# Performance work log

Measured on AMD Instinct MI355X. Metric: run time of the kernel, lower is better.

Reference implementation:

```python
import jax, jax.numpy as jnp
import numpy as np

EPS = 1e-5  # haiku LayerNorm default
BIG = 1e9


def layernorm(x, scale, offset):
    mu = jnp.mean(x, axis=-1, keepdims=True)
    var = jnp.var(x, axis=-1, keepdims=True)
    return scale * (x - mu) * jax.lax.rsqrt(var + EPS) + offset


def setup_inputs() -> dict:
    key = jax.random.key(0)
    ks = iter(jax.random.split(key, 32))
    N_res, N_tok, C, H = 4096, 512, 384, 8
    kd = C // H  # 48, key_dim and value_dim per head
    F = 4 * C    # transition hidden
    s = 0.02
    inp = {
        "original": jax.random.normal(next(ks), (1, N_res, C), jnp.float32),
        "resampled": jax.random.normal(next(ks), (1, N_tok, C), jnp.float32),
        "attention_mask": (jax.random.uniform(next(ks), (H, N_tok, N_res)) < 0.9).astype(jnp.float32),
        "output_mask": jnp.ones((1, N_tok), jnp.float32),
        "input_mask": jnp.ones((1, N_res), jnp.float32),
        # cross-attention LayerNorms
        "qn_scale": jnp.ones((C,), jnp.float32), "qn_offset": jnp.zeros((C,), jnp.float32),
        "dn_scale": jnp.ones((C,), jnp.float32), "dn_offset": jnp.zeros((C,), jnp.float32),
        # attention projections
        "query_w": jax.random.normal(next(ks), (C, H, kd), jnp.float32) * s,
        "key_w": jax.random.normal(next(ks), (C, H, kd), jnp.float32) * s,
        "value_w": jax.random.normal(next(ks), (C, H, kd), jnp.float32) * s,
        "gating_w": jax.random.normal(next(ks), (C, H, kd), jnp.float32) * s,
        "gating_b": jnp.ones((H, kd), jnp.float32),
        "output_w": jax.random.normal(next(ks), (H, kd, C), jnp.float32) * s,
        "output_b": jnp.zeros((C,), jnp.float32),
        # resampled transition
        "rt_ln_scale": jnp.ones((C,), jnp.float32), "rt_ln_offset": jnp.zeros((C,), jnp.float32),
        "rt_w1": jax.random.normal(next(ks), (C, F), jnp.float32) * s, "rt_b1": jnp.zeros((F,), jnp.float32),
        "rt_w2": jax.random.normal(next(ks), (F, C), jnp.float32) * s, "rt_b2": jnp.zeros((C,), jnp.float32),
        # original transition
        "ot_ln_scale": jnp.ones((C,), jnp.float32), "ot_ln_offset": jnp.zeros((C,), jnp.float32),
        "ot_w1": jax.random.normal(next(ks), (C, F), jnp.float32) * s, "ot_b1": jnp.zeros((F,), jnp.float32),
        "ot_w2": jax.random.normal(next(ks), (F, C), jnp.float32) * s, "ot_b2": jnp.zeros((C,), jnp.float32),
    }
    return inp


def reference(original, resampled, attention_mask, output_mask, input_mask,
              qn_scale, qn_offset, dn_scale, dn_offset,
              query_w, key_w, value_w, gating_w, gating_b, output_w, output_b,
              rt_ln_scale, rt_ln_offset, rt_w1, rt_b1, rt_w2, rt_b2,
              ot_ln_scale, ot_ln_offset, ot_w1, ot_b1, ot_w2, ot_b2):
    # ---- CrossAttention (deterministic; dropout rate 0) ----
    bias = BIG * (attention_mask - 1.0)          # [H, T, R]
    q_in = layernorm(resampled, qn_scale, qn_offset)   # [1, T, C]
    d_in = layernorm(original, dn_scale, dn_offset)    # [1, R, C]
    kd = query_w.shape[-1]
    q = jnp.einsum('bqa,ahc->bqhc', q_in, query_w) * kd ** (-0.5)
    k = jnp.einsum('bka,ahc->bkhc', d_in, key_w)
    v = jnp.einsum('bka,ahc->bkhc', d_in, value_w)
    logits = jnp.einsum('bqhc,bkhc->bhqk', q, k) + bias[None]  # [1, H, T, R]
    weights = jax.nn.softmax(logits, axis=-1)
    weighted_avg = jnp.einsum('bhqk,bkhc->bqhc', weights, v)
    gate = jax.nn.sigmoid(jnp.einsum('bqc,chv->bqhv', q_in, gating_w) + gating_b)
    weighted_avg = weighted_avg * gate
    attn_out = jnp.einsum('bqhc,hco->bqo', weighted_avg, output_w) + output_b
    resampled = resampled + attn_out             # residual (dropout off)
    # ---- resampled Transition + residual ----
    t = layernorm(resampled, rt_ln_scale, rt_ln_offset)
    t = jax.nn.relu(t @ rt_w1 + rt_b1) @ rt_w2 + rt_b2
    resampled = resampled + t
    # ---- original Transition + residual ----
    t = layernorm(original, ot_ln_scale, ot_ln_offset)
    t = jax.nn.relu(t @ ot_w1 + ot_b1) @ ot_w2 + ot_b2
    original = original + t
    return resampled.astype(jnp.float32), original.astype(jnp.float32)
```

## Files before the change

kernel.cpp:

```cpp
#include <hip/hip_runtime.h>
#include <hip/hip_bf16.h>
#include <cstdint>

typedef unsigned short u16;
typedef __attribute__((ext_vector_type(8))) __bf16 bf16x8;
typedef __attribute__((ext_vector_type(4))) float f32x4;
typedef __attribute__((ext_vector_type(4))) short s16x4;

__device__ __forceinline__ u16 f2bf(float f) {
  union { float f; unsigned u; } v; v.f = f;
  unsigned r = (v.u + 0x7FFFu + ((v.u >> 16) & 1u)) >> 16;
  return (u16)r;
}

__device__ __forceinline__ void gll16(const u16* gp, u16* lp) {
  auto g1 = reinterpret_cast<const __attribute__((address_space(1))) void*>(
      reinterpret_cast<uintptr_t>(gp));
  auto l3 = reinterpret_cast<__attribute__((address_space(3))) void*>(
      reinterpret_cast<uintptr_t>(lp));
  __builtin_amdgcn_global_load_lds(g1, l3, 16, 0, 0);
}

__global__ __launch_bounds__(128) void ln_kernel(
    const float* __restrict__ x,
    const float* __restrict__ s1, const float* __restrict__ o1, u16* __restrict__ y1,
    const float* __restrict__ s2, const float* __restrict__ o2, u16* __restrict__ y2) {
  const int row = blockIdx.x;
  const int t = threadIdx.x;
  const float* xr = x + (size_t)row * 384;
  float v0 = xr[t], v1 = xr[t + 128], v2 = xr[t + 256];
  float sum = v0 + v1 + v2;
  float sq = v0 * v0 + v1 * v1 + v2 * v2;
#pragma unroll
  for (int off = 32; off > 0; off >>= 1) {
    sum += __shfl_xor(sum, off);
    sq += __shfl_xor(sq, off);
  }
  __shared__ float red[4];
  if ((t & 63) == 0) { red[(t >> 6) * 2] = sum; red[(t >> 6) * 2 + 1] = sq; }
  __syncthreads();
  sum = red[0] + red[2];
  sq = red[1] + red[3];
  const float mu = sum * (1.f / 384.f);
  const float rstd = rsqrtf(sq * (1.f / 384.f) - mu * mu + 1e-5f);
#pragma unroll
  for (int j = 0; j < 3; ++j) {
    const int cc = t + 128 * j;
    const float xv = (j == 0 ? v0 : (j == 1 ? v1 : v2));
    const float xn = (xv - mu) * rstd;
    y1[(size_t)row * 384 + cc] = f2bf(s1[cc] * xn + o1[cc]);
    if (y2) y2[(size_t)row * 384 + cc] = f2bf(s2[cc] * xn + o2[cc]);
  }
}

struct TBatch {
  const float* in[9];
  u16* out[9];
  int K[9], N[9];
  float scale[9];
  int boff[10];
};

__global__ __launch_bounds__(256) void transpose_all(TBatch tb) {
  __shared__ float tile[32][33];
  const int bid = blockIdx.x;
  int j = 0;
  while (j < 8 && bid >= tb.boff[j + 1]) ++j;
  const int lb = bid - tb.boff[j];
  const int NB = tb.N[j] >> 5;
  const int bx = lb % NB, by = lb / NB;
  const float* in = tb.in[j];
  u16* out = tb.out[j];
  const int K = tb.K[j], N = tb.N[j];
  const float scale = tb.scale[j];
  const int tx = threadIdx.x, ty = threadIdx.y;
  const int nb = bx * 32, kb = by * 32;
#pragma unroll
  for (int i = 0; i < 4; ++i)
    tile[ty + 8 * i][tx] = in[(size_t)(kb + ty + 8 * i) * N + nb + tx];
  __syncthreads();
#pragma unroll
  for (int i = 0; i < 4; ++i)
    out[(size_t)(nb + ty + 8 * i) * K + kb + tx] = f2bf(tile[tx][ty + 8 * i] * scale);
}

struct GArgs {
  const u16* A; const u16* Bt;
  int M, N, K;
  const float* bias; const float* bias2; const float* residual;
  float* outf; u16* outb; u16* outb2;
};

template <int BM, int BN, int EPI>
__global__ __launch_bounds__(256, (BM == 128 ? 2 : 4)) void gemm_bt(GArgs g) {
  constexpr int MT = BM / 32, NT = BN / 32;
  const int tid = threadIdx.x;
  const int w = tid >> 6;
  const int lane = tid & 63;
  const int gq = lane >> 4, c = lane & 15;
  const int brow = blockIdx.y * BM, bcol = blockIdx.x * BN;
  const int wm = (w >> 1) * (BM / 2), wn = (w & 1) * (BN / 2);
  __shared__ u16 As[2][BM][64];
  __shared__ u16 Bs[2][BN][64];
  const int K = g.K;

  f32x4 acc[MT][NT];
#pragma unroll
  for (int mt = 0; mt < MT; ++mt)
#pragma unroll
    for (int nt = 0; nt < NT; ++nt)
#pragma unroll
      for (int r = 0; r < 4; ++r) acc[mt][nt][r] = 0.f;

  const int srow = lane >> 3;
  const int schunk = (lane & 7) ^ srow;
  const u16* aSrc = g.A + (size_t)(brow + w * (BM / 4) + srow) * K + schunk * 8;
  const u16* bSrc = g.Bt + (size_t)(bcol + w * (BN / 4) + srow) * K + schunk * 8;

  auto STAGE = [&](int buf, int k0) {
#pragma unroll
    for (int i = 0; i < BM / 32; ++i)
      gll16(aSrc + (size_t)(8 * i) * K + k0, &As[buf][w * (BM / 4) + i * 8][0]);
#pragma unroll
    for (int i = 0; i < BN / 32; ++i)
      gll16(bSrc + (size_t)(8 * i) * K + k0, &Bs[buf][w * (BN / 4) + i * 8][0]);
  };

  auto COMPUTE = [&](int buf) {
#pragma unroll
    for (int ks = 0; ks < 2; ++ks) {
      bf16x8 af[MT], bfv[NT];
#pragma unroll
      for (int mt = 0; mt < MT; ++mt) {
        const int row = wm + mt * 16 + c;
        const int ch = ((ks << 2) | gq) ^ (row & 7);
        af[mt] = *(const bf16x8*)&As[buf][row][ch * 8];
      }
#pragma unroll
      for (int nt = 0; nt < NT; ++nt) {
        const int row = wn + nt * 16 + c;
        const int ch = ((ks << 2) | gq) ^ (row & 7);
        bfv[nt] = *(const bf16x8*)&Bs[buf][row][ch * 8];
      }
#pragma unroll
      for (int mt = 0; mt < MT; ++mt)
#pragma unroll
        for (int nt = 0; nt < NT; ++nt)
          acc[mt][nt] =
              __builtin_amdgcn_mfma_f32_16x16x32_bf16(af[mt], bfv[nt], acc[mt][nt], 0, 0, 0);
    }
  };

  const int NTILES = K >> 6;
  STAGE(0, 0);
  __syncthreads();
  int cur = 0;
  for (int t = 0; t < NTILES; ++t) {
    if (t + 1 < NTILES) STAGE(cur ^ 1, (t + 1) << 6);
    COMPUTE(cur);
    __syncthreads();
    cur ^= 1;
  }

  const int N = g.N;
#pragma unroll
  for (int mt = 0; mt < MT; ++mt) {
#pragma unroll
    for (int nt = 0; nt < NT; ++nt) {
      const int n = bcol + wn + nt * 16 + c;
#pragma unroll
      for (int r = 0; r < 4; ++r) {
        const int m = brow + wm + mt * 16 + 4 * gq + r;
        const float v = acc[mt][nt][r];
        if (EPI == 0) {
          g.outb[(size_t)m * N + n] = f2bf(fmaxf(v + g.bias[n], 0.f));
        } else if (EPI == 1) {
          g.outf[(size_t)m * N + n] = v + g.bias[n] + g.residual[(size_t)m * N + n];
        } else if (EPI == 2) {
          if (n < 384) g.outb[(size_t)(n / 48) * 4096 * 48 + (size_t)m * 48 + (n % 48)] = f2bf(v);
          else g.outb2[(size_t)(n - 384) * 4096 + m] = f2bf(v);
        } else {
          if (n < 384) g.outb[(size_t)m * 384 + n] = f2bf(v);
          else {
            const float sg = v + g.bias2[n - 384];
            g.outf[(size_t)m * 384 + (n - 384)] = 1.f / (1.f + __expf(-sg));
          }
        }
      }
    }
  }
}

__global__ __launch_bounds__(512) void attn_kernel(
    const u16* __restrict__ Kh, const u16* __restrict__ Qb, const u16* __restrict__ Vt,
    const float* __restrict__ mask, float* __restrict__ partO, float* __restrict__ partL) {
  const int tid = threadIdx.x;
  const int w = tid >> 6;
  const int lane = tid & 63;
  const int gq = lane >> 4, c = lane & 15;
  const int qt = blockIdx.x, h = blockIdx.y, z = blockIdx.z;
  const int tb = qt * 16;

  bf16x8 zf;
#pragma unroll
  for (int j = 0; j < 8; ++j) zf[j] = (__bf16)0.f;
  f32x4 zero4;
#pragma unroll
  for (int j = 0; j < 4; ++j) zero4[j] = 0.f;

  const u16* qrow = Qb + (size_t)(tb + c) * 384 + h * 48;
  bf16x8 qf0 = *(const bf16x8*)(qrow + 8 * gq);
  bf16x8 qf1 = zf;
  if (gq < 2) qf1 = *(const bf16x8*)(qrow + 32 + 8 * gq);

  float psum = 0.f;
  f32x4 O0 = zero4, O1 = zero4, O2 = zero4;

  const int kb = z * 1024 + w * 128;
  const float* mrow = mask + ((size_t)h * 512 + tb + c) * 4096;
  const u16* khead = Kh + (size_t)h * 4096 * 48;
  const u16* vbase = Vt + (size_t)(h * 48) * 4096;

#pragma unroll
  for (int it = 0; it < 4; ++it) {
    const int rb = kb + it * 32;
    const u16* krow0 = khead + (size_t)(rb + c) * 48;
    const u16* krow1 = krow0 + (size_t)16 * 48;

    bf16x8 kf0a = *(const bf16x8*)(krow0 + 8 * gq);
    bf16x8 kf0b = zf;
    if (gq < 2) kf0b = *(const bf16x8*)(krow0 + 32 + 8 * gq);
    bf16x8 kf1a = *(const bf16x8*)(krow1 + 8 * gq);
    bf16x8 kf1b = zf;
    if (gq < 2) kf1b = *(const bf16x8*)(krow1 + 32 + 8 * gq);

    f32x4 s0 = __builtin_amdgcn_mfma_f32_16x16x32_bf16(kf0a, qf0, zero4, 0, 0, 0);
    s0 = __builtin_amdgcn_mfma_f32_16x16x32_bf16(kf0b, qf1, s0, 0, 0, 0);
    f32x4 s1 = __builtin_amdgcn_mfma_f32_16x16x32_bf16(kf1a, qf0, zero4, 0, 0, 0);
    s1 = __builtin_amdgcn_mfma_f32_16x16x32_bf16(kf1b, qf1, s1, 0, 0, 0);

    const f32x4 mv0 = *(const f32x4*)(mrow + rb + 4 * gq);
    const f32x4 mv1 = *(const f32x4*)(mrow + rb + 16 + 4 * gq);

    float p0[4], p1[4];
#pragma unroll
    for (int r = 0; r < 4; ++r) {
      p0[r] = __expf(s0[r] + 1e9f * (mv0[r] - 1.f));
      p1[r] = __expf(s1[r] + 1e9f * (mv1[r] - 1.f));
      psum += p0[r] + p1[r];
    }

    s16x4 pa0, pa1;
#pragma unroll
    for (int r = 0; r < 4; ++r) {
      pa0[r] = (short)f2bf(p0[r]);
      pa1[r] = (short)f2bf(p1[r]);
    }
#pragma unroll
    for (int nt = 0; nt < 3; ++nt) {
      const u16* vp = vbase + (size_t)(nt * 16 + c) * 4096 + rb + 4 * gq;
      const s16x4 vf0 = *(const s16x4*)(vp);
      const s16x4 vf1 = *(const s16x4*)(vp + 16);
      f32x4& O = (nt == 0 ? O0 : (nt == 1 ? O1 : O2));
      O = __builtin_amdgcn_mfma_f32_16x16x16bf16_1k(pa0, vf0, O, 0, 0, 0);
      O = __builtin_amdgcn_mfma_f32_16x16x16bf16_1k(pa1, vf1, O, 0, 0, 0);
    }
  }

  psum += __shfl_xor(psum, 16);
  psum += __shfl_xor(psum, 32);

  __shared__ float oS[8][16][48];
  __shared__ float lS[8][16];
  if (gq == 0) lS[w][c] = psum;
#pragma unroll
  for (int r = 0; r < 4; ++r) {
    oS[w][4 * gq + r][c] = O0[r];
    oS[w][4 * gq + r][16 + c] = O1[r];
    oS[w][4 * gq + r][32 + c] = O2[r];
  }
  __syncthreads();

  float* pO = partO + (((size_t)z * 32 + qt) * 8 + h) * 768;
  for (int idx = tid; idx < 768; idx += 512) {
    const int q = idx / 48, d = idx % 48;
    float v = 0.f;
#pragma unroll
    for (int ww = 0; ww < 8; ++ww) v += oS[ww][q][d];
    pO[idx] = v;
  }
  if (tid < 16) {
    float L = 0.f;
#pragma unroll
    for (int ww = 0; ww < 8; ++ww) L += lS[ww][tid];
    partL[(((size_t)z * 32 + qt) * 8 + h) * 16 + tid] = L;
  }
}

__global__ __launch_bounds__(256) void attn_merge(
    const float* __restrict__ partO, const float* __restrict__ partL,
    const float* __restrict__ gate, u16* __restrict__ attng) {
  const int qt = blockIdx.x, h = blockIdx.y;
  for (int idx = threadIdx.x; idx < 768; idx += 256) {
    const int q = idx / 48, d = idx % 48;
    float O = 0.f, L = 0.f;
#pragma unroll
    for (int z = 0; z < 4; ++z) {
      O += partO[(((size_t)z * 32 + qt) * 8 + h) * 768 + idx];
      L += partL[(((size_t)z * 32 + qt) * 8 + h) * 16 + q];
    }
    const size_t off = (size_t)(qt * 16 + q) * 384 + h * 48 + d;
    attng[off] = f2bf(O / L * gate[off]);
  }
}

extern "C" void kernel_launch(void* const* d_in, const int* in_sizes, int n_in,
                              void* d_out, int out_size, void* d_ws, size_t ws_size,
                              hipStream_t stream) {
  (void)in_sizes; (void)n_in; (void)out_size; (void)ws_size;
  const float* original = (const float*)d_in[0];
  const float* resampled = (const float*)d_in[1];
  const float* amask = (const float*)d_in[2];
  const float* qn_s = (const float*)d_in[5];
  const float* qn_o = (const float*)d_in[6];
  const float* dn_s = (const float*)d_in[7];
  const float* dn_o = (const float*)d_in[8];
  const float* w_q = (const float*)d_in[9];
  const float* w_k = (const float*)d_in[10];
  const float* w_v = (const float*)d_in[11];
  const float* w_g = (const float*)d_in[12];
  const float* b_g = (const float*)d_in[13];
  const float* w_o = (const float*)d_in[14];
  const float* b_o = (const float*)d_in[15];
  const float* rt_s = (const float*)d_in[16];
  const float* rt_o = (const float*)d_in[17];
  const float* rtw1 = (const float*)d_in[18];
  const float* rtb1 = (const float*)d_in[19];
  const float* rtw2 = (const float*)d_in[20];
  const float* rtb2 = (const float*)d_in[21];
  const float* ot_s = (const float*)d_in[22];
  const float* ot_o = (const float*)d_in[23];
  const float* otw1 = (const float*)d_in[24];
  const float* otb1 = (const float*)d_in[25];
  const float* otw2 = (const float*)d_in[26];
  const float* otb2 = (const float*)d_in[27];

  float* out_res = (float*)d_out;
  float* out_orig = out_res + 512 * 384;

  char* p = (char*)d_ws;
  auto alloc = [&](size_t n) {
    void* r = (void*)p;
    p += (n + 255) & ~(size_t)255;
    return r;
  };
  u16* dinb = (u16*)alloc(4096 * 384 * 2);
  u16* otin = (u16*)alloc(4096 * 384 * 2);
  u16* qin = (u16*)alloc(512 * 384 * 2);
  u16* Kh = (u16*)alloc((size_t)8 * 4096 * 48 * 2);
  u16* Vt = (u16*)alloc(384 * 4096 * 2);
  u16* Qb = (u16*)alloc(512 * 384 * 2);
  float* gateb = (float*)alloc(512 * 384 * 4);
  u16* attng = (u16*)alloc(512 * 384 * 2);
  float* res2 = (float*)alloc(512 * 384 * 4);
  u16* tin = (u16*)alloc(512 * 384 * 2);
  u16* H1 = (u16*)alloc(512 * 1536 * 2);
  u16* H2 = (u16*)alloc((size_t)4096 * 1536 * 2);
  u16* BtKV = (u16*)alloc(768 * 384 * 2);
  u16* BtQG = (u16*)alloc(768 * 384 * 2);
  u16* OwT = (u16*)alloc(384 * 384 * 2);
  u16* Rt1T = (u16*)alloc(1536 * 384 * 2);
  u16* Rt2T = (u16*)alloc(384 * 1536 * 2);
  u16* Ot1T = (u16*)alloc(1536 * 384 * 2);
  u16* Ot2T = (u16*)alloc(384 * 1536 * 2);
  float* partO = (float*)alloc((size_t)4 * 32 * 8 * 768 * 4);
  float* partL = (float*)alloc((size_t)4 * 32 * 8 * 16 * 4);

  {
    TBatch tb{};
    const float qscale = 0.14433756729740643f;
    const float* ins[9] = {w_q, w_g, w_k, w_v, w_o, rtw1, rtw2, otw1, otw2};
    u16* outs[9] = {BtQG, BtQG + 384 * 384, BtKV, BtKV + 384 * 384, OwT,
                    Rt1T, Rt2T, Ot1T, Ot2T};
    const int Ks[9] = {384, 384, 384, 384, 384, 384, 1536, 384, 1536};
    const int Ns[9] = {384, 384, 384, 384, 384, 1536, 384, 1536, 384};
    int off = 0;
    for (int j = 0; j < 9; ++j) {
      tb.in[j] = ins[j]; tb.out[j] = outs[j];
      tb.K[j] = Ks[j]; tb.N[j] = Ns[j];
      tb.scale[j] = (j == 0) ? qscale : 1.f;
      tb.boff[j] = off;
      off += (Ns[j] >> 5) * (Ks[j] >> 5);
    }
    tb.boff[9] = off;
    transpose_all<<<off, dim3(32, 8), 0, stream>>>(tb);
  }

  ln_kernel<<<4096, 128, 0, stream>>>(original, dn_s, dn_o, dinb, ot_s, ot_o, otin);
  ln_kernel<<<512, 128, 0, stream>>>(resampled, qn_s, qn_o, qin, nullptr, nullptr, nullptr);

  {
    GArgs a{};
    a.A = dinb; a.Bt = BtKV; a.M = 4096; a.N = 768; a.K = 384;
    a.outb = Kh; a.outb2 = Vt;
    gemm_bt<128, 128, 2><<<dim3(6, 32), 256, 0, stream>>>(a);
  }
  {
    GArgs a{};
    a.A = qin; a.Bt = BtQG; a.M = 512; a.N = 768; a.K = 384;
    a.outb = Qb; a.outf = gateb; a.bias2 = b_g;
    gemm_bt<64, 64, 3><<<dim3(12, 8), 256, 0, stream>>>(a);
  }

  attn_kernel<<<dim3(32, 8, 4), 512, 0, stream>>>(Kh, Qb, Vt, amask, partO, partL);
  attn_merge<<<dim3(32, 8), 256, 0, stream>>>(partO, partL, gateb, attng);

  {
    GArgs a{};
    a.A = attng; a.Bt = OwT; a.M = 512; a.N = 384; a.K = 384;
    a.bias = b_o; a.residual = resampled; a.outf = res2;
    gemm_bt<64, 64, 1><<<dim3(6, 8), 256, 0, stream>>>(a);
  }
  ln_kernel<<<512, 128, 0, stream>>>(res2, rt_s, rt_o, tin, nullptr, nullptr, nullptr);
  {
    GArgs a{};
    a.A = tin; a.Bt = Rt1T; a.M = 512; a.N = 1536; a.K = 384;
    a.bias = rtb1; a.outb = H1;
    gemm_bt<64, 64, 0><<<dim3(24, 8), 256, 0, stream>>>(a);
  }
  {
    GArgs a{};
    a.A = H1; a.Bt = Rt2T; a.M = 512; a.N = 384; a.K = 1536;
    a.bias = rtb2; a.residual = res2; a.outf = out_res;
    gemm_bt<64, 64, 1><<<dim3(6, 8), 256, 0, stream>>>(a);
  }
  {
    GArgs a{};
    a.A = otin; a.Bt = Ot1T; a.M = 4096; a.N = 1536; a.K = 384;
    a.bias = otb1; a.outb = H2;
    gemm_bt<128, 128, 0><<<dim3(12, 32), 256, 0, stream>>>(a);
  }
  {
    GArgs a{};
    a.A = H2; a.Bt = Ot2T; a.M = 4096; a.N = 384; a.K = 1536;
    a.bias = otb2; a.residual = original; a.outf = out_orig;
    gemm_bt<64, 64, 1><<<dim3(6, 64), 256, 0, stream>>>(a);
  }
}
```

Measured before the change: 292.2 us.

## Split-K FFN down-projections, pad K/Q heads, and restructure attention into 8-way key split

Merges the two input LayerNorm launches into one kernel. Pads K and Q per-head storage to 64 columns, with a memset providing zeros, so the attention kernel drops its conditional half-loads. It also strides V rows by 4160 to avoid bank/channel aliasing. The attention kernel moves to 256 threads with 8 key splits, software-pipelines its loads across iterations, and turns the mask into a multiply on exp instead of a large negative bias. Both transition down-projection GEMMs become split-K with a fused merge kernel that adds bias and residual, raising parallelism at the cost of extra fp32 partial traffic and a memset.

```diff
diff --git a/kernel.cpp b/kernel.cpp
--- a/kernel.cpp
+++ b/kernel.cpp
@@ -6,6 +6,8 @@
 typedef __attribute__((ext_vector_type(8))) __bf16 bf16x8;
 typedef __attribute__((ext_vector_type(4))) float f32x4;
 typedef __attribute__((ext_vector_type(4))) short s16x4;
+
+#define VSTR 4160
 
 __device__ __forceinline__ u16 f2bf(float f) {
   union { float f; unsigned u; } v; v.f = f;
@@ -21,13 +23,15 @@
   __builtin_amdgcn_global_load_lds(g1, l3, 16, 0, 0);
 }
 
-__global__ __launch_bounds__(128) void ln_kernel(
-    const float* __restrict__ x,
-    const float* __restrict__ s1, const float* __restrict__ o1, u16* __restrict__ y1,
-    const float* __restrict__ s2, const float* __restrict__ o2, u16* __restrict__ y2) {
+__global__ __launch_bounds__(128) void ln_all(
+    const float* __restrict__ orig, const float* __restrict__ resam,
+    const float* __restrict__ dn_s, const float* __restrict__ dn_o, u16* __restrict__ dinb,
+    const float* __restrict__ ot_s, const float* __restrict__ ot_o, u16* __restrict__ otin,
+    const float* __restrict__ qn_s, const float* __restrict__ qn_o, u16* __restrict__ qin) {
   const int row = blockIdx.x;
   const int t = threadIdx.x;
-  const float* xr = x + (size_t)row * 384;
+  const bool isOrig = row < 4096;
+  const float* xr = isOrig ? orig + (size_t)row * 384 : resam + (size_t)(row - 4096) * 384;
   float v0 = xr[t], v1 = xr[t + 128], v2 = xr[t + 256];
   float sum = v0 + v1 + v2;
   float sq = v0 * v0 + v1 * v1 + v2 * v2;
@@ -48,8 +52,41 @@
     const int cc = t + 128 * j;
     const float xv = (j == 0 ? v0 : (j == 1 ? v1 : v2));
     const float xn = (xv - mu) * rstd;
-    y1[(size_t)row * 384 + cc] = f2bf(s1[cc] * xn + o1[cc]);
-    if (y2) y2[(size_t)row * 384 + cc] = f2bf(s2[cc] * xn + o2[cc]);
+    if (isOrig) {
+      dinb[(size_t)row * 384 + cc] = f2bf(dn_s[cc] * xn + dn_o[cc]);
+      otin[(size_t)row * 384 + cc] = f2bf(ot_s[cc] * xn + ot_o[cc]);
+    } else {
+      qin[(size_t)(row - 4096) * 384 + cc] = f2bf(qn_s[cc] * xn + qn_o[cc]);
+    }
+  }
+}
+
+__global__ __launch_bounds__(128) void ln_kernel(
+    const float* __restrict__ x,
+    const float* __restrict__ s1, const float* __restrict__ o1, u16* __restrict__ y1) {
+  const int row = blockIdx.x;
+  const int t = threadIdx.x;
+  const float* xr = x + (size_t)row * 384;
+  float v0 = xr[t], v1 = xr[t + 128], v2 = xr[t + 256];
+  float sum = v0 + v1 + v2;
+  float sq = v0 * v0 + v1 * v1 + v2 * v2;
+#pragma unroll
+  for (int off = 32; off > 0; off >>= 1) {
+    sum += __shfl_xor(sum, off);
+    sq += __shfl_xor(sq, off);
+  }
+  __shared__ float red[4];
+  if ((t & 63) == 0) { red[(t >> 6) * 2] = sum; red[(t >> 6) * 2 + 1] = sq; }
+  __syncthreads();
+  sum = red[0] + red[2];
+  sq = red[1] + red[3];
+  const float mu = sum * (1.f / 384.f);
+  const float rstd = rsqrtf(sq * (1.f / 384.f) - mu * mu + 1e-5f);
+#pragma unroll
+  for (int j = 0; j < 3; ++j) {
+    const int cc = t + 128 * j;
+    const float xv = (j == 0 ? v0 : (j == 1 ? v1 : v2));
+    y1[(size_t)row * 384 + cc] = f2bf(s1[cc] * ((xv - mu) * rstd) + o1[cc]);
   }
 }
 
@@ -86,7 +123,7 @@
 
 struct GArgs {
   const u16* A; const u16* Bt;
-  int M, N, K;
+  int M, N, K, Kld;
   const float* bias; const float* bias2; const float* residual;
   float* outf; u16* outb; u16* outb2;
 };
@@ -103,6 +140,8 @@
   __shared__ u16 As[2][BM][64];
   __shared__ u16 Bs[2][BN][64];
   const int K = g.K;
+  const int Kld = g.Kld;
+  const size_t koff = (size_t)blockIdx.z * K;
 
   f32x4 acc[MT][NT];
 #pragma unroll
@@ -114,16 +153,16 @@
 
   const int srow = lane >> 3;
   const int schunk = (lane & 7) ^ srow;
-  const u16* aSrc = g.A + (size_t)(brow + w * (BM / 4) + srow) * K + schunk * 8;
-  const u16* bSrc = g.Bt + (size_t)(bcol + w * (BN / 4) + srow) * K + schunk * 8;
+  const u16* aSrc = g.A + (size_t)(brow + w * (BM / 4) + srow) * Kld + koff + schunk * 8;
+  const u16* bSrc = g.Bt + (size_t)(bcol + w * (BN / 4) + srow) * Kld + koff + schunk * 8;
 
   auto STAGE = [&](int buf, int k0) {
 #pragma unroll
     for (int i = 0; i < BM / 32; ++i)
-      gll16(aSrc + (size_t)(8 * i) * K + k0, &As[buf][w * (BM / 4) + i * 8][0]);
+      gll16(aSrc + (size_t)(8 * i) * Kld + k0, &As[buf][w * (BM / 4) + i * 8][0]);
 #pragma unroll
     for (int i = 0; i < BN / 32; ++i)
-      gll16(bSrc + (size_t)(8 * i) * K + k0, &Bs[buf][w * (BN / 4) + i * 8][0]);
+      gll16(bSrc + (size_t)(8 * i) * Kld + k0, &Bs[buf][w * (BN / 4) + i * 8][0]);
   };
 
   auto COMPUTE = [&](int buf) {
@@ -177,21 +216,89 @@
         } else if (EPI == 1) {
           g.outf[(size_t)m * N + n] = v + g.bias[n] + g.residual[(size_t)m * N + n];
         } else if (EPI == 2) {
-          if (n < 384) g.outb[(size_t)(n / 48) * 4096 * 48 + (size_t)m * 48 + (n % 48)] = f2bf(v);
-          else g.outb2[(size_t)(n - 384) * 4096 + m] = f2bf(v);
-        } else {
-          if (n < 384) g.outb[(size_t)m * 384 + n] = f2bf(v);
+          if (n < 384)
+            g.outb[(size_t)(n / 48) * 4096 * 64 + (size_t)m * 64 + (n % 48)] = f2bf(v);
+          else
+            g.outb2[(size_t)(n - 384) * VSTR + m] = f2bf(v);
+        } else if (EPI == 3) {
+          if (n < 384)
+            g.outb[(size_t)(n / 48) * 512 * 64 + (size_t)m * 64 + (n % 48)] = f2bf(v);
           else {
             const float sg = v + g.bias2[n - 384];
             g.outf[(size_t)m * 384 + (n - 384)] = 1.f / (1.f + __expf(-sg));
           }
+        } else {
+          g.outf[(size_t)blockIdx.z * g.M * N + (size_t)m * N + n] = v;
         }
       }
     }
   }
 }
 
-__global__ __launch_bounds__(512) void attn_kernel(
+struct KIter {
+  bf16x8 kA0, kA1, kB0, kB1;
+  f32x4 mv0, mv1;
+  s16x4 v0, v1, v2, v3, v4, v5;
+};
+
+__device__ __forceinline__ KIter load_iter(const u16* __restrict__ khead,
+                                           const float* __restrict__ mrow,
+                                           const u16* __restrict__ vcol, int rb) {
+  KIter I;
+  const u16* kr = khead + (size_t)rb * 64;
+  I.kA0 = *(const bf16x8*)(kr);
+  I.kA1 = *(const bf16x8*)(kr + 32);
+  I.kB0 = *(const bf16x8*)(kr + 16 * 64);
+  I.kB1 = *(const bf16x8*)(kr + 16 * 64 + 32);
+  I.mv0 = *(const f32x4*)(mrow + rb);
+  I.mv1 = *(const f32x4*)(mrow + rb + 16);
+  const u16* vp0 = vcol + rb;
+  I.v0 = *(const s16x4*)(vp0);
+  I.v1 = *(const s16x4*)(vp0 + 16);
+  const u16* vp1 = vp0 + (size_t)16 * VSTR;
+  I.v2 = *(const s16x4*)(vp1);
+  I.v3 = *(const s16x4*)(vp1 + 16);
+  const u16* vp2 = vp1 + (size_t)16 * VSTR;
+  I.v4 = *(const s16x4*)(vp2);
+  I.v5 = *(const s16x4*)(vp2 + 16);
+  return I;
+}
+
+__device__ __forceinline__ void comp_iter(const KIter& I, const bf16x8& qf0,
+                                          const bf16x8& qf1, f32x4& O0, f32x4& O1,
+                                          f32x4& O2, float& psum) {
+  f32x4 z4;
+#pragma unroll
+  for (int r = 0; r < 4; ++r) z4[r] = 0.f;
+  f32x4 s0 = __builtin_amdgcn_mfma_f32_16x16x32_bf16(I.kA0, qf0, z4, 0, 0, 0);
+  s0 = __builtin_amdgcn_mfma_f32_16x16x32_bf16(I.kA1, qf1, s0, 0, 0, 0);
+  f32x4 s1 = __builtin_amdgcn_mfma_f32_16x16x32_bf16(I.kB0, qf0, z4, 0, 0, 0);
+  s1 = __builtin_amdgcn_mfma_f32_16x16x32_bf16(I.kB1, qf1, s1, 0, 0, 0);
+  float p0[4], p1[4];
+#pragma unroll
+  for (int r = 0; r < 4; ++r) {
+    p0[r] = I.mv0[r] * __expf(s0[r]);
+    p1[r] = I.mv1[r] * __expf(s1[r]);
+    psum += p0[r] + p1[r];
+  }
+  s16x4 pa0, pa1;
+  ((unsigned*)&pa0)[0] = __builtin_amdgcn_perm(__builtin_bit_cast(unsigned, p0[1]),
+                                               __builtin_bit_cast(unsigned, p0[0]), 0x07060302u);
+  ((unsigned*)&pa0)[1] = __builtin_amdgcn_perm(__builtin_bit_cast(unsigned, p0[3]),
+                                               __builtin_bit_cast(unsigned, p0[2]), 0x07060302u);
+  ((unsigned*)&pa1)[0] = __builtin_amdgcn_perm(__builtin_bit_cast(unsigned, p1[1]),
+                                               __builtin_bit_cast(unsigned, p1[0]), 0x07060302u);
+  ((unsigned*)&pa1)[1] = __builtin_amdgcn_perm(__builtin_bit_cast(unsigned, p1[3]),
+                                               __builtin_bit_cast(unsigned, p1[2]), 0x07060302u);
+  O0 = __builtin_amdgcn_mfma_f32_16x16x16bf16_1k(pa0, I.v0, O0, 0, 0, 0);
+  O0 = __builtin_amdgcn_mfma_f32_16x16x16bf16_1k(pa1, I.v1, O0, 0, 0, 0);
+  O1 = __builtin_amdgcn_mfma_f32_16x16x16bf16_1k(pa0, I.v2, O1, 0, 0, 0);
+  O1 = __builtin_amdgcn_mfma_f32_16x16x16bf16_1k(pa1, I.v3, O1, 0, 0, 0);
+  O2 = __builtin_amdgcn_mfma_f32_16x16x16bf16_1k(pa0, I.v4, O2, 0, 0, 0);
+  O2 = __builtin_amdgcn_mfma_f32_16x16x16bf16_1k(pa1, I.v5, O2, 0, 0, 0);
+}
+
+__global__ __launch_bounds__(256, 3) void attn_kernel(
     const u16* __restrict__ Kh, const u16* __restrict__ Qb, const u16* __restrict__ Vt,
     const float* __restrict__ mask, float* __restrict__ partO, float* __restrict__ partL) {
   const int tid = threadIdx.x;
@@ -200,78 +307,35 @@
   const int gq = lane >> 4, c = lane & 15;
   const int qt = blockIdx.x, h = blockIdx.y, z = blockIdx.z;
   const int tb = qt * 16;
-
-  bf16x8 zf;
-#pragma unroll
-  for (int j = 0; j < 8; ++j) zf[j] = (__bf16)0.f;
-  f32x4 zero4;
-#pragma unroll
-  for (int j = 0; j < 4; ++j) zero4[j] = 0.f;
-
-  const u16* qrow = Qb + (size_t)(tb + c) * 384 + h * 48;
-  bf16x8 qf0 = *(const bf16x8*)(qrow + 8 * gq);
-  bf16x8 qf1 = zf;
-  if (gq < 2) qf1 = *(const bf16x8*)(qrow + 32 + 8 * gq);
-
+  const int kb = z * 512 + w * 128;
+
+  const u16* qrow = Qb + ((size_t)h * 512 + tb + c) * 64;
+  const bf16x8 qf0 = *(const bf16x8*)(qrow + 8 * gq);
+  const bf16x8 qf1 = *(const bf16x8*)(qrow + 32 + 8 * gq);
+
+  const u16* khead = Kh + (size_t)h * 4096 * 64 + (size_t)c * 64 + 8 * gq;
+  const float* mrow = mask + ((size_t)h * 512 + tb + c) * 4096 + 4 * gq;
+  const u16* vcol = Vt + ((size_t)h * 48 + c) * VSTR + 4 * gq;
+
+  f32x4 O0, O1, O2;
+#pragma unroll
+  for (int r = 0; r < 4; ++r) { O0[r] = 0.f; O1[r] = 0.f; O2[r] = 0.f; }
   float psum = 0.f;
-  f32x4 O0 = zero4, O1 = zero4, O2 = zero4;
-
-  const int kb = z * 1024 + w * 128;
-  const float* mrow = mask + ((size_t)h * 512 + tb + c) * 4096;
-  const u16* khead = Kh + (size_t)h * 4096 * 48;
-  const u16* vbase = Vt + (size_t)(h * 48) * 4096;
-
-#pragma unroll
-  for (int it = 0; it < 4; ++it) {
-    const int rb = kb + it * 32;
-    const u16* krow0 = khead + (size_t)(rb + c) * 48;
-    const u16* krow1 = krow0 + (size_t)16 * 48;
-
-    bf16x8 kf0a = *(const bf16x8*)(krow0 + 8 * gq);
-    bf16x8 kf0b = zf;
-    if (gq < 2) kf0b = *(const bf16x8*)(krow0 + 32 + 8 * gq);
-    bf16x8 kf1a = *(const bf16x8*)(krow1 + 8 * gq);
-    bf16x8 kf1b = zf;
-    if (gq < 2) kf1b = *(const bf16x8*)(krow1 + 32 + 8 * gq);
-
-    f32x4 s0 = __builtin_amdgcn_mfma_f32_16x16x32_bf16(kf0a, qf0, zero4, 0, 0, 0);
-    s0 = __builtin_amdgcn_mfma_f32_16x16x32_bf16(kf0b, qf1, s0, 0, 0, 0);
-    f32x4 s1 = __builtin_amdgcn_mfma_f32_16x16x32_bf16(kf1a, qf0, zero4, 0, 0, 0);
-    s1 = __builtin_amdgcn_mfma_f32_16x16x32_bf16(kf1b, qf1, s1, 0, 0, 0);
-
-    const f32x4 mv0 = *(const f32x4*)(mrow + rb + 4 * gq);
-    const f32x4 mv1 = *(const f32x4*)(mrow + rb + 16 + 4 * gq);
-
-    float p0[4], p1[4];
-#pragma unroll
-    for (int r = 0; r < 4; ++r) {
-      p0[r] = __expf(s0[r] + 1e9f * (mv0[r] - 1.f));
-      p1[r] = __expf(s1[r] + 1e9f * (mv1[r] - 1.f));
-      psum += p0[r] + p1[r];
-    }
-
-    s16x4 pa0, pa1;
-#pragma unroll
-    for (int r = 0; r < 4; ++r) {
-      pa0[r] = (short)f2bf(p0[r]);
-      pa1[r] = (short)f2bf(p1[r]);
-    }
-#pragma unroll
-    for (int nt = 0; nt < 3; ++nt) {
-      const u16* vp = vbase + (size_t)(nt * 16 + c) * 4096 + rb + 4 * gq;
-      const s16x4 vf0 = *(const s16x4*)(vp);
-      const s16x4 vf1 = *(const s16x4*)(vp + 16);
-      f32x4& O = (nt == 0 ? O0 : (nt == 1 ? O1 : O2));
-      O = __builtin_amdgcn_mfma_f32_16x16x16bf16_1k(pa0, vf0, O, 0, 0, 0);
-      O = __builtin_amdgcn_mfma_f32_16x16x16bf16_1k(pa1, vf1, O, 0, 0, 0);
-    }
-  }
+
+  KIter Ia = load_iter(khead, mrow, vcol, kb);
+  KIter Ib = load_iter(khead, mrow, vcol, kb + 32);
+  comp_iter(Ia, qf0, qf1, O0, O1, O2, psum);
+  Ia = load_iter(khead, mrow, vcol, kb + 64);
+  comp_iter(Ib, qf0, qf1, O0, O1, O2, psum);
+  Ib = load_iter(khead, mrow, vcol, kb + 96);
+  comp_iter(Ia, qf0, qf1, O0, O1, O2, psum);
+  comp_iter(Ib, qf0, qf1, O0, O1, O2, psum);
 
   psum += __shfl_xor(psum, 16);
   psum += __shfl_xor(psum, 32);
 
-  __shared__ float oS[8][16][48];
-  __shared__ float lS[8][16];
+  __shared__ float oS[4][16][48];
+  __shared__ float lS[4][16];
   if (gq == 0) lS[w][c] = psum;
 #pragma unroll
   for (int r = 0; r < 4; ++r) {
@@ -282,17 +346,17 @@
   __syncthreads();
 
   float* pO = partO + (((size_t)z * 32 + qt) * 8 + h) * 768;
-  for (int idx = tid; idx < 768; idx += 512) {
+  for (int idx = tid; idx < 768; idx += 256) {
     const int q = idx / 48, d = idx % 48;
     float v = 0.f;
 #pragma unroll
-    for (int ww = 0; ww < 8; ++ww) v += oS[ww][q][d];
+    for (int ww = 0; ww < 4; ++ww) v += oS[ww][q][d];
     pO[idx] = v;
   }
   if (tid < 16) {
     float L = 0.f;
 #pragma unroll
-    for (int ww = 0; ww < 8; ++ww) L += lS[ww][tid];
+    for (int ww = 0; ww < 4; ++ww) L += lS[ww][tid];
     partL[(((size_t)z * 32 + qt) * 8 + h) * 16 + tid] = L;
   }
 }
@@ -305,12 +369,50 @@
     const int q = idx / 48, d = idx % 48;
     float O = 0.f, L = 0.f;
 #pragma unroll
-    for (int z = 0; z < 4; ++z) {
+    for (int z = 0; z < 8; ++z) {
       O += partO[(((size_t)z * 32 + qt) * 8 + h) * 768 + idx];
       L += partL[(((size_t)z * 32 + qt) * 8 + h) * 16 + q];
     }
     const size_t off = (size_t)(qt * 16 + q) * 384 + h * 48 + d;
     attng[off] = f2bf(O / L * gate[off]);
+  }
+}
+
+__global__ __launch_bounds__(256) void fmerge(
+    const float* __restrict__ pT1, const float* __restrict__ res2,
+    const float* __restrict__ rtb2, float* __restrict__ out_res,
+    const float* __restrict__ pT2, const float* __restrict__ orig,
+    const float* __restrict__ otb2, float* __restrict__ out_orig) {
+  const int NT1 = 512 * 384 / 4;
+  const int NT2 = 4096 * 384 / 4;
+  const int i = blockIdx.x * 256 + threadIdx.x;
+  if (i < NT1) {
+    const int n0 = (i * 4) % 384;
+    f32x4 v = *(const f32x4*)(res2 + (size_t)i * 4);
+#pragma unroll
+    for (int z = 0; z < 4; ++z) {
+      const f32x4 pz = *(const f32x4*)(pT1 + (size_t)z * 512 * 384 + (size_t)i * 4);
+#pragma unroll
+      for (int r = 0; r < 4; ++r) v[r] += pz[r];
+    }
+    const f32x4 b = *(const f32x4*)(rtb2 + n0);
+#pragma unroll
+    for (int r = 0; r < 4; ++r) v[r] += b[r];
+    *(f32x4*)(out_res + (size_t)i * 4) = v;
+  } else if (i < NT1 + NT2) {
+    const int j = i - NT1;
+    const int n0 = (j * 4) % 384;
+    f32x4 v = *(const f32x4*)(orig + (size_t)j * 4);
+#pragma unroll
+    for (int z = 0; z < 2; ++z) {
+      const f32x4 pz = *(const f32x4*)(pT2 + (size_t)z * 4096 * 384 + (size_t)j * 4);
+#pragma unroll
+      for (int r = 0; r < 4; ++r) v[r] += pz[r];
+    }
+    const f32x4 b = *(const f32x4*)(otb2 + n0);
+#pragma unroll
+    for (int r = 0; r < 4; ++r) v[r] += b[r];
+    *(f32x4*)(out_orig + (size_t)j * 4) = v;
   }
 }
 
@@ -354,18 +456,22 @@
     p += (n + 255) & ~(size_t)255;
     return r;
   };
+  u16* Kh = (u16*)alloc((size_t)8 * 4096 * 64 * 2);
+  u16* Qb = (u16*)alloc((size_t)8 * 512 * 64 * 2);
   u16* dinb = (u16*)alloc(4096 * 384 * 2);
   u16* otin = (u16*)alloc(4096 * 384 * 2);
   u16* qin = (u16*)alloc(512 * 384 * 2);
-  u16* Kh = (u16*)alloc((size_t)8 * 4096 * 48 * 2);
-  u16* Vt = (u16*)alloc(384 * 4096 * 2);
-  u16* Qb = (u16*)alloc(512 * 384 * 2);
+  u16* Vt = (u16*)alloc((size_t)384 * VSTR * 2);
   float* gateb = (float*)alloc(512 * 384 * 4);
   u16* attng = (u16*)alloc(512 * 384 * 2);
   float* res2 = (float*)alloc(512 * 384 * 4);
   u16* tin = (u16*)alloc(512 * 384 * 2);
   u16* H1 = (u16*)alloc(512 * 1536 * 2);
   u16* H2 = (u16*)alloc((size_t)4096 * 1536 * 2);
+  float* partT1 = (float*)alloc((size_t)4 * 512 * 384 * 4);
+  float* partT2 = (float*)alloc((size_t)2 * 4096 * 384 * 4);
+  float* partO = partT2;
+  float* partL = partT2 + (size_t)8 * 32 * 8 * 768;
   u16* BtKV = (u16*)alloc(768 * 384 * 2);
   u16* BtQG = (u16*)alloc(768 * 384 * 2);
   u16* OwT = (u16*)alloc(384 * 384 * 2);
@@ -373,8 +479,8 @@
   u16* Rt2T = (u16*)alloc(384 * 1536 * 2);
   u16* Ot1T = (u16*)alloc(1536 * 384 * 2);
   u16* Ot2T = (u16*)alloc(384 * 1536 * 2);
-  float* partO = (float*)alloc((size_t)4 * 32 * 8 * 768 * 4);
-  float* partL = (float*)alloc((size_t)4 * 32 * 8 * 16 * 4);
+
+  hipMemsetAsync(Kh, 0, (size_t)8 * 4096 * 64 * 2 + (size_t)8 * 512 * 64 * 2, stream);
 
   {
     TBatch tb{};
@@ -396,54 +502,56 @@
     transpose_all<<<off, dim3(32, 8), 0, stream>>>(tb);
   }
 
-  ln_kernel<<<4096, 128, 0, stream>>>(original, dn_s, dn_o, dinb, ot_s, ot_o, otin);
-  ln_kernel<<<512, 128, 0, stream>>>(resampled, qn_s, qn_o, qin, nullptr, nullptr, nullptr);
-
-  {
-    GArgs a{};
-    a.A = dinb; a.Bt = BtKV; a.M = 4096; a.N = 768; a.K = 384;
+  ln_all<<<4608, 128, 0, stream>>>(original, resampled, dn_s, dn_o, dinb,
+                                   ot_s, ot_o, otin, qn_s, qn_o, qin);
+
+  {
+    GArgs a{};
+    a.A = dinb; a.Bt = BtKV; a.M = 4096; a.N = 768; a.K = 384; a.Kld = 384;
     a.outb = Kh; a.outb2 = Vt;
     gemm_bt<128, 128, 2><<<dim3(6, 32), 256, 0, stream>>>(a);
   }
   {
     GArgs a{};
-    a.A = qin; a.Bt = BtQG; a.M = 512; a.N = 768; a.K = 384;
+    a.A = qin; a.Bt = BtQG; a.M = 512; a.N = 768; a.K = 384; a.Kld = 384;
     a.outb = Qb; a.outf = gateb; a.bias2 = b_g;
     gemm_bt<64, 64, 3><<<dim3(12, 8), 256, 0, stream>>>(a);
   }
 
-  attn_kernel<<<dim3(32, 8, 4), 512, 0, stream>>>(Kh, Qb, Vt, amask, partO, partL);
+  attn_kernel<<<dim3(32, 8, 8), 256, 0, stream>>>(Kh, Qb, Vt, amask, partO, partL);
   attn_merge<<<dim3(32, 8), 256, 0, stream>>>(partO, partL, gateb, attng);
 
   {
     GArgs a{};
-    a.A = attng; a.Bt = OwT; a.M = 512; a.N = 384; a.K = 384;
+    a.A = attng; a.Bt = OwT; a.M = 512; a.N = 384; a.K = 384; a.Kld = 384;
     a.bias = b_o; a.residual = resampled; a.outf = res2;
     gemm_bt<64, 64, 1><<<dim3(6, 8), 256, 0, stream>>>(a);
   }
-  ln_kernel<<<512, 128, 0, stream>>>(res2, rt_s, rt_o, tin, nullptr, nullptr, nullptr);
-  {
-    GArgs a{};
-    a.A = tin; a.Bt = Rt1T; a.M = 512; a.N = 1536; a.K = 384;
+  ln_kernel<<<512, 128, 0, stream>>>(res2, rt_s, rt_o, tin);
+  {
+    GArgs a{};
+    a.A = tin; a.Bt = Rt1T; a.M = 512; a.N = 1536; a.K = 384; a.Kld = 384;
     a.bias = rtb1; a.outb = H1;
     gemm_bt<64, 64, 0><<<dim3(24, 8), 256, 0, stream>>>(a);
   }
   {
     GArgs a{};
-    a.A = H1; a.Bt = Rt2T; a.M = 512; a.N = 384; a.K = 1536;
-    a.bias = rtb2; a.residual = res2; a.outf = out_res;
-    gemm_bt<64, 64, 1><<<dim3(6, 8), 256, 0, stream>>>(a);
-  }
-  {
-    GArgs a{};
-    a.A = otin; a.Bt = Ot1T; a.M = 4096; a.N = 1536; a.K = 384;
+    a.A = H1; a.Bt = Rt2T; a.M = 512; a.N = 384; a.K = 384; a.Kld = 1536;
+    a.outf = partT1;
+    gemm_bt<64, 64, 4><<<dim3(6, 8, 4), 256, 0, stream>>>(a);
+  }
+  {
+    GArgs a{};
+    a.A = otin; a.Bt = Ot1T; a.M = 4096; a.N = 1536; a.K = 384; a.Kld = 384;
     a.bias = otb1; a.outb = H2;
     gemm_bt<128, 128, 0><<<dim3(12, 32), 256, 0, stream>>>(a);
   }
   {
     GArgs a{};
-    a.A = H2; a.Bt = Ot2T; a.M = 4096; a.N = 384; a.K = 1536;
-    a.bias = otb2; a.residual = original; a.outf = out_orig;
-    gemm_bt<64, 64, 1><<<dim3(6, 64), 256, 0, stream>>>(a);
-  }
-}
+    a.A = H2; a.Bt = Ot2T; a.M = 4096; a.N = 384; a.K = 768; a.Kld = 1536;
+    a.outf = partT2;
+    gemm_bt<64, 64, 4><<<dim3(6, 64, 2), 256, 0, stream>>>(a);
+  }
+  fmerge<<<(512 * 384 / 4 + 4096 * 384 / 4 + 255) / 256, 256, 0, stream>>>(
+      partT1, res2, rtb2, out_res, partT2, original, otb2, out_orig);
+}
```

After: 289.1 us. No clear change (-1.1%).
